# Kernel tuning notes

Measured on AMD Instinct MI355X. Metric: run time of the kernel, lower is better.

## Reference

```python
import jax, jax.numpy as jnp
import numpy as np

N, E, RBF_DIM, DIM = 50000, 800000, 128, 64
BETA, THRESH = 0.5, 14.0


def softplus_b05(x):
    # torch Softplus(beta=0.5, threshold=14): (1/beta)*log1p(exp(beta*x)) if beta*x<=14 else x
    z = BETA * x
    safe = jnp.where(z > THRESH, 0.0, z)
    return jnp.where(z > THRESH, x, (1.0 / BETA) * jnp.log1p(jnp.exp(safe)))


def setup_inputs() -> dict:
    key = jax.random.key(0)
    ks = jax.random.split(key, 10)
    s = 0.02
    return {
        "new_node": jax.random.normal(ks[0], (N, DIM), jnp.float32),
        "rbf": jax.random.normal(ks[1], (E, RBF_DIM), jnp.float32),
        "edge_f": jax.random.normal(ks[2], (E, DIM), jnp.float32),
        "src": jax.random.randint(ks[3], (E,), 0, N, jnp.int32),
        "dst": jax.random.randint(ks[4], (E,), 0, N, jnp.int32),
        "W1": jax.random.normal(ks[5], (RBF_DIM, DIM), jnp.float32) * s,
        "b1": jnp.zeros((DIM,), jnp.float32),
        "W2": jax.random.normal(ks[6], (DIM, DIM), jnp.float32) * s,
        "b2": jnp.zeros((DIM,), jnp.float32),
        "W3": jax.random.normal(ks[7], (DIM, DIM), jnp.float32) * s,
        "b3": jnp.zeros((DIM,), jnp.float32),
    }


def reference(new_node, rbf, edge_f, src, dst, W1, b1, W2, b2, W3, b3):
    # per-edge MLP on RBF features: h = L2(softplus(L1(rbf)))  [E, DIM]
    h = softplus_b05(rbf @ W1 + b1) @ W2 + b2
    # edge embedding update: edge_f' = L3(edge_f)  [E, DIM]
    edge_f_new = edge_f @ W3 + b3
    # messages: m0 = new_node[src] * h (u_mul_e), m1 = edge_f' (copy_e)
    m = new_node[src] * h + edge_f_new
    # sum-reduce messages at destination nodes
    out = jax.ops.segment_sum(m, dst, num_segments=N)  # [N, DIM]
    return out
```

## Files before the change

kernel.cpp:

```cpp
#include <hip/hip_runtime.h>
#include <hip/hip_bf16.h>
#include <math.h>


typedef __bf16 bf16x8 __attribute__((ext_vector_type(8)));
typedef float f32x4 __attribute__((ext_vector_type(4)));

#define RBF_DIM 128
#define DIM 64

__global__ __launch_bounds__(256) void veconv_kernel(
    const float* __restrict__ new_node,
    const float* __restrict__ rbf,
    const float* __restrict__ edge_f,
    const int* __restrict__ src,
    const int* __restrict__ dst,
    const float* __restrict__ W1, const float* __restrict__ b1,
    const float* __restrict__ W2, const float* __restrict__ b2,
    const float* __restrict__ W3, const float* __restrict__ b3,
    float* __restrict__ out, int N, int E)
{
    __shared__ __align__(16) unsigned char lds[40960];
    unsigned char* w1t = lds;
    unsigned char* w2t = lds + 16384;
    unsigned char* w3t = lds + 24576;

    const int tid = threadIdx.x;
    const int w   = tid >> 6;
    const int l   = tid & 63;
    unsigned char* actw = lds + 32768 + (w << 11);

    for (int idx = tid; idx < RBF_DIM * DIM; idx += 256) {
        int k = idx >> 6, n = idx & 63;
        unsigned off = ((((unsigned)n) << 8) + (((unsigned)k) << 1)) ^ (((unsigned)(n & 7)) << 4);
        *(__bf16*)(w1t + off) = (__bf16)W1[idx];
    }
    for (int idx = tid; idx < DIM * DIM; idx += 256) {
        int k = idx >> 6, n = idx & 63;
        unsigned off = ((((unsigned)n) << 7) + (((unsigned)k) << 1)) ^ (((unsigned)(n & 7)) << 4);
        *(__bf16*)(w2t + off) = (__bf16)W2[idx];
        *(__bf16*)(w3t + off) = (__bf16)W3[idx];
    }
    __syncthreads();

    const int l15 = l & 15;
    const int q   = l >> 4;
    const unsigned sw = ((unsigned)(l & 7)) << 4;

    float b1v[4], b2v[4], b3v[4];
    #pragma unroll
    for (int nt = 0; nt < 4; ++nt) {
        b1v[nt] = b1[l15 + (nt << 4)];
        b2v[nt] = b2[l15 + (nt << 4)];
        b3v[nt] = b3[l15 + (nt << 4)];
    }

    const int NT = E >> 6;

    for (int t = blockIdx.x; t < NT; t += gridDim.x) {
        const int ebase = (t << 6) + (w << 4);

        const float* rrow = rbf + (size_t)(ebase + l15) * RBF_DIM + (q << 3);
        bf16x8 a1[4];
        #pragma unroll
        for (int kc = 0; kc < 4; ++kc) {
            const float4 u = *(const float4*)(rrow + kc * 32);
            const float4 v = *(const float4*)(rrow + kc * 32 + 4);
            bf16x8 a;
            a[0] = (__bf16)u.x; a[1] = (__bf16)u.y; a[2] = (__bf16)u.z; a[3] = (__bf16)u.w;
            a[4] = (__bf16)v.x; a[5] = (__bf16)v.y; a[6] = (__bf16)v.z; a[7] = (__bf16)v.w;
            a1[kc] = a;
        }

        f32x4 acc1[4] = {{0.f,0.f,0.f,0.f},{0.f,0.f,0.f,0.f},{0.f,0.f,0.f,0.f},{0.f,0.f,0.f,0.f}};
        #pragma unroll
        for (int kc = 0; kc < 4; ++kc) {
            #pragma unroll
            for (int nt = 0; nt < 4; ++nt) {
                unsigned off = ((((unsigned)(l15 + (nt << 4))) << 8) + ((unsigned)kc << 6) + ((unsigned)q << 4)) ^ sw;
                bf16x8 bf = *(const bf16x8*)(w1t + off);
                acc1[nt] = __builtin_amdgcn_mfma_f32_16x16x32_bf16(a1[kc], bf, acc1[nt], 0, 0, 0);
            }
        }

        #pragma unroll
        for (int nt = 0; nt < 4; ++nt) {
            #pragma unroll
            for (int i = 0; i < 4; ++i) {
                float x = acc1[nt][i] + b1v[nt];
                float z = 0.5f * x;
                float s = (z > 14.0f) ? x : 2.0f * log1pf(__expf(z));
                int e = (q << 2) + i;
                int d = l15 + (nt << 4);
                unsigned off = ((((unsigned)e) << 7) + (((unsigned)d) << 1)) ^ (((unsigned)(e & 7)) << 4);
                *(__bf16*)(actw + off) = (__bf16)s;
            }
        }
        __syncthreads();

        bf16x8 a2[2];
        #pragma unroll
        for (int kc = 0; kc < 2; ++kc) {
            unsigned off = ((((unsigned)l15) << 7) + ((unsigned)kc << 6) + ((unsigned)q << 4)) ^ sw;
            a2[kc] = *(const bf16x8*)(actw + off);
        }

        const float* erow = edge_f + (size_t)(ebase + l15) * DIM + (q << 3);
        bf16x8 a3[2];
        #pragma unroll
        for (int kc = 0; kc < 2; ++kc) {
            const float4 u = *(const float4*)(erow + kc * 32);
            const float4 v = *(const float4*)(erow + kc * 32 + 4);
            bf16x8 a;
            a[0] = (__bf16)u.x; a[1] = (__bf16)u.y; a[2] = (__bf16)u.z; a[3] = (__bf16)u.w;
            a[4] = (__bf16)v.x; a[5] = (__bf16)v.y; a[6] = (__bf16)v.z; a[7] = (__bf16)v.w;
            a3[kc] = a;
        }

        f32x4 acc2[4] = {{0.f,0.f,0.f,0.f},{0.f,0.f,0.f,0.f},{0.f,0.f,0.f,0.f},{0.f,0.f,0.f,0.f}};
        f32x4 acc3[4] = {{0.f,0.f,0.f,0.f},{0.f,0.f,0.f,0.f},{0.f,0.f,0.f,0.f},{0.f,0.f,0.f,0.f}};
        #pragma unroll
        for (int kc = 0; kc < 2; ++kc) {
            #pragma unroll
            for (int nt = 0; nt < 4; ++nt) {
                unsigned boff = ((((unsigned)(l15 + (nt << 4))) << 7) + ((unsigned)kc << 6) + ((unsigned)q << 4)) ^ sw;
                bf16x8 bf2 = *(const bf16x8*)(w2t + boff);
                bf16x8 bf3 = *(const bf16x8*)(w3t + boff);
                acc2[nt] = __builtin_amdgcn_mfma_f32_16x16x32_bf16(a2[kc], bf2, acc2[nt], 0, 0, 0);
                acc3[nt] = __builtin_amdgcn_mfma_f32_16x16x32_bf16(a3[kc], bf3, acc3[nt], 0, 0, 0);
            }
        }

        const int4 s4 = *(const int4*)(src + ebase + (q << 2));
        const int4 d4 = *(const int4*)(dst + ebase + (q << 2));
        const int sa[4] = {s4.x, s4.y, s4.z, s4.w};
        const int da[4] = {d4.x, d4.y, d4.z, d4.w};
        #pragma unroll
        for (int i = 0; i < 4; ++i) {
            #pragma unroll
            for (int nt = 0; nt < 4; ++nt) {
                int d = l15 + (nt << 4);
                float nv = new_node[sa[i] * DIM + d];
                float mv = fmaf(nv, acc2[nt][i] + b2v[nt], acc3[nt][i] + b3v[nt]);
                atomicAdd(out + (size_t)da[i] * DIM + d, mv);
            }
        }
    }
}

extern "C" void kernel_launch(void* const* d_in, const int* in_sizes, int n_in,
                              void* d_out, int out_size, void* d_ws, size_t ws_size,
                              hipStream_t stream) {
    const float* new_node = (const float*)d_in[0];
    const float* rbf      = (const float*)d_in[1];
    const float* edge_f   = (const float*)d_in[2];
    const int*   src      = (const int*)d_in[3];
    const int*   dst      = (const int*)d_in[4];
    const float* W1 = (const float*)d_in[5];
    const float* b1 = (const float*)d_in[6];
    const float* W2 = (const float*)d_in[7];
    const float* b2 = (const float*)d_in[8];
    const float* W3 = (const float*)d_in[9];
    const float* b3 = (const float*)d_in[10];
    float* out = (float*)d_out;

    const int E = in_sizes[3];
    const int N = in_sizes[0] / DIM;

    hipMemsetAsync(d_out, 0, (size_t)out_size * sizeof(float), stream);

    veconv_kernel<<<dim3(1024), dim3(256), 0, stream>>>(
        new_node, rbf, edge_f, src, dst, W1, b1, W2, b2, W3, b3, out, N, E);
}
```

Measured before the change: 928.6 us.

## Hoist all global loads to loop top, drop block barrier, use fast log

Moves the rbf, edge_f, src/dst and new_node gather loads to the start of each tile iteration so their latency overlaps the first MFMA stage. The per-tile __syncthreads is replaced by a wave-local LDS waitcnt, since each wave only reads back its own activation region. log1pf is replaced with __logf(1+e^z), which is cheaper but less accurate for small arguments. Holding more loaded values live raises register pressure and may lower occupancy.

Result: faster. 760.9 us (-18.1%).

```diff
diff --git a/kernel.cpp b/kernel.cpp
--- a/kernel.cpp
+++ b/kernel.cpp
@@ -60,16 +60,41 @@
     for (int t = blockIdx.x; t < NT; t += gridDim.x) {
         const int ebase = (t << 6) + (w << 4);
 
+        const int4 s4 = *(const int4*)(src + ebase + (q << 2));
+        const int4 d4 = *(const int4*)(dst + ebase + (q << 2));
+
         const float* rrow = rbf + (size_t)(ebase + l15) * RBF_DIM + (q << 3);
+        float4 rv[8];
+        #pragma unroll
+        for (int c = 0; c < 4; ++c) {
+            rv[2*c]   = *(const float4*)(rrow + c * 32);
+            rv[2*c+1] = *(const float4*)(rrow + c * 32 + 4);
+        }
+        const float* erow = edge_f + (size_t)(ebase + l15) * DIM + (q << 3);
+        float4 ev[4];
+        #pragma unroll
+        for (int c = 0; c < 2; ++c) {
+            ev[2*c]   = *(const float4*)(erow + c * 32);
+            ev[2*c+1] = *(const float4*)(erow + c * 32 + 4);
+        }
+
+        const int sa[4] = {s4.x, s4.y, s4.z, s4.w};
+        const int da[4] = {d4.x, d4.y, d4.z, d4.w};
+        float nv[4][4];
+        #pragma unroll
+        for (int i = 0; i < 4; ++i)
+            #pragma unroll
+            for (int nt = 0; nt < 4; ++nt)
+                nv[i][nt] = new_node[(size_t)sa[i] * DIM + l15 + (nt << 4)];
+
         bf16x8 a1[4];
         #pragma unroll
-        for (int kc = 0; kc < 4; ++kc) {
-            const float4 u = *(const float4*)(rrow + kc * 32);
-            const float4 v = *(const float4*)(rrow + kc * 32 + 4);
+        for (int c = 0; c < 4; ++c) {
+            const float4 u = rv[2*c], v = rv[2*c+1];
             bf16x8 a;
             a[0] = (__bf16)u.x; a[1] = (__bf16)u.y; a[2] = (__bf16)u.z; a[3] = (__bf16)u.w;
             a[4] = (__bf16)v.x; a[5] = (__bf16)v.y; a[6] = (__bf16)v.z; a[7] = (__bf16)v.w;
-            a1[kc] = a;
+            a1[c] = a;
         }
 
         f32x4 acc1[4] = {{0.f,0.f,0.f,0.f},{0.f,0.f,0.f,0.f},{0.f,0.f,0.f,0.f},{0.f,0.f,0.f,0.f}};
@@ -89,14 +114,15 @@
             for (int i = 0; i < 4; ++i) {
                 float x = acc1[nt][i] + b1v[nt];
                 float z = 0.5f * x;
-                float s = (z > 14.0f) ? x : 2.0f * log1pf(__expf(z));
+                float ez = __expf(z);
+                float s = (z > 14.0f) ? x : 2.0f * __logf(1.0f + ez);
                 int e = (q << 2) + i;
                 int d = l15 + (nt << 4);
                 unsigned off = ((((unsigned)e) << 7) + (((unsigned)d) << 1)) ^ (((unsigned)(e & 7)) << 4);
                 *(__bf16*)(actw + off) = (__bf16)s;
             }
         }
-        __syncthreads();
+        asm volatile("s_waitcnt lgkmcnt(0)" ::: "memory");
 
         bf16x8 a2[2];
         #pragma unroll
@@ -105,16 +131,14 @@
             a2[kc] = *(const bf16x8*)(actw + off);
         }
 
-        const float* erow = edge_f + (size_t)(ebase + l15) * DIM + (q << 3);
         bf16x8 a3[2];
         #pragma unroll
-        for (int kc = 0; kc < 2; ++kc) {
-            const float4 u = *(const float4*)(erow + kc * 32);
-            const float4 v = *(const float4*)(erow + kc * 32 + 4);
+        for (int c = 0; c < 2; ++c) {
+            const float4 u = ev[2*c], v = ev[2*c+1];
             bf16x8 a;
             a[0] = (__bf16)u.x; a[1] = (__bf16)u.y; a[2] = (__bf16)u.z; a[3] = (__bf16)u.w;
             a[4] = (__bf16)v.x; a[5] = (__bf16)v.y; a[6] = (__bf16)v.z; a[7] = (__bf16)v.w;
-            a3[kc] = a;
+            a3[c] = a;
         }
 
         f32x4 acc2[4] = {{0.f,0.f,0.f,0.f},{0.f,0.f,0.f,0.f},{0.f,0.f,0.f,0.f},{0.f,0.f,0.f,0.f}};
@@ -131,17 +155,12 @@
             }
         }
 
-        const int4 s4 = *(const int4*)(src + ebase + (q << 2));
-        const int4 d4 = *(const int4*)(dst + ebase + (q << 2));
-        const int sa[4] = {s4.x, s4.y, s4.z, s4.w};
-        const int da[4] = {d4.x, d4.y, d4.z, d4.w};
         #pragma unroll
         for (int i = 0; i < 4; ++i) {
             #pragma unroll
             for (int nt = 0; nt < 4; ++nt) {
                 int d = l15 + (nt << 4);
-                float nv = new_node[sa[i] * DIM + d];
-                float mv = fmaf(nv, acc2[nt][i] + b2v[nt], acc3[nt][i] + b3v[nt]);
+                float mv = fmaf(nv[i][nt], acc2[nt][i] + b2v[nt], acc3[nt][i] + b3v[nt]);
                 atomicAdd(out + (size_t)da[i] * DIM + d, mv);
             }
         }
```
